# Kernel tuning notes

Measured on AMD Instinct MI355X. Metric: run time of the kernel, lower is better.

The kernel has to match this reference:

```python
import jax, jax.numpy as jnp
from jax import lax
import numpy as np

B, H, W = 8, 36, 100  # stride-8 feature map of 288x800 input
PAD = 4               # ms_ks // 2 for ms_ks = 9
EPS = 1e-5
FC_IN = 5 * (800 // 16) * (288 // 16)  # 4500


def setup_inputs() -> dict:
    key = jax.random.key(0)
    ks = jax.random.split(key, 12)
    r = lambda k, s, sc: jax.random.normal(k, s, jnp.float32) * sc
    return {
        "x": jax.random.normal(ks[0], (B, 512, H, W), jnp.float32),
        "w1a": r(ks[1], (1024, 512, 3, 3), 0.02),
        "bn1_g": jnp.ones(1024, jnp.float32), "bn1_b": jnp.zeros(1024, jnp.float32),
        "bn1_m": jnp.zeros(1024, jnp.float32), "bn1_v": jnp.ones(1024, jnp.float32),
        "w1b": r(ks[2], (128, 1024, 1, 1), 0.03),
        "bn2_g": jnp.ones(128, jnp.float32), "bn2_b": jnp.zeros(128, jnp.float32),
        "bn2_m": jnp.zeros(128, jnp.float32), "bn2_v": jnp.ones(128, jnp.float32),
        "w_ud": r(ks[3], (128, 128, 9), 0.02),
        "w_du": r(ks[4], (128, 128, 9), 0.02),
        "w_lr": r(ks[5], (128, 128, 9), 0.02),
        "w_rl": r(ks[6], (128, 128, 9), 0.02),
        "w2": r(ks[7], (5, 128, 1, 1), 0.05), "b2": jnp.zeros(5, jnp.float32),
        "fc1_w": r(ks[8], (128, FC_IN), 0.02), "fc1_b": jnp.zeros(128, jnp.float32),
        "fc2_w": r(ks[9], (4, 128), 0.05), "fc2_b": jnp.zeros(4, jnp.float32),
    }


def bn(x, g, b, m, v):
    s = (g / jnp.sqrt(v + EPS))
    return x * s[None, :, None, None] + (b - m * s)[None, :, None, None]


def conv2d(x, w, padding, dilation=(1, 1)):
    return lax.conv_general_dilated(x, w, (1, 1), padding, rhs_dilation=dilation,
                                    dimension_numbers=("NCHW", "OIHW", "NCHW"))


def conv1d(x, w):  # x [B,C,L], w [O,I,K]
    return lax.conv_general_dilated(x, w, (1,), [(PAD, PAD)],
                                    dimension_numbers=("NCH", "OIH", "NCH"))


def message_pass(x, w, axis, reverse):
    # x [B,C,H,W]; scan over `axis`, 1D conv along the other spatial dim
    xs = jnp.moveaxis(x, axis, 0)  # [L, B, C, other]
    if reverse:
        xs = xs[::-1]

    def step(prev, cur):
        new = cur + jax.nn.relu(conv1d(prev, w))
        return new, new

    first = xs[0]
    _, rest = lax.scan(step, first, xs[1:])
    out = jnp.concatenate([first[None], rest], axis=0)
    if reverse:
        out = out[::-1]
    return jnp.moveaxis(out, 0, axis)


def upsample_bilinear_ac(x, scale):
    # align_corners=True bilinear, NCHW
    b, c, h, w = x.shape
    ho, wo = h * scale, w * scale

    def grid(n_in, n_out):
        pos = jnp.arange(n_out, dtype=x.dtype) * ((n_in - 1) / (n_out - 1))
        i0 = jnp.clip(jnp.floor(pos).astype(jnp.int32), 0, n_in - 2)
        return i0, pos - i0.astype(x.dtype)

    i0, fh = grid(h, ho)
    j0, fw = grid(w, wo)
    xh = x[:, :, i0, :] * (1 - fh)[None, None, :, None] + x[:, :, i0 + 1, :] * fh[None, None, :, None]
    return xh[:, :, :, j0] * (1 - fw)[None, None, None, :] + xh[:, :, :, j0 + 1] * fw[None, None, None, :]


def reference(x, w1a, bn1_g, bn1_b, bn1_m, bn1_v, w1b, bn2_g, bn2_b, bn2_m, bn2_v,
              w_ud, w_du, w_lr, w_rl, w2, b2, fc1_w, fc1_b, fc2_w, fc2_b):
    # layer1: dilated 3x3 (pad=4, dil=4) -> BN -> ReLU -> 1x1 -> BN -> ReLU
    h = jax.nn.relu(bn(conv2d(x, w1a, [(4, 4), (4, 4)], dilation=(4, 4)), bn1_g, bn1_b, bn1_m, bn1_v))
    h = jax.nn.relu(bn(conv2d(h, w1b, [(0, 0), (0, 0)]), bn2_g, bn2_b, bn2_m, bn2_v))
    # message passing: up-down, down-up (vertical), left-right, right-left (horizontal)
    h = message_pass(h, w_ud, axis=2, reverse=False)
    h = message_pass(h, w_du, axis=2, reverse=True)
    h = message_pass(h, w_lr, axis=3, reverse=False)
    h = message_pass(h, w_rl, axis=3, reverse=True)
    # layer2 (Dropout2d is identity at eval): 1x1 conv -> 5 channels
    h = conv2d(h, w2, [(0, 0), (0, 0)]) + b2[None, :, None, None]
    seg_pred = upsample_bilinear_ac(h, 8)  # [B,5,288,800]
    # layer3: softmax over channels, then AvgPool2d(2,2)
    p = jax.nn.softmax(h, axis=1)
    b_, c_, hh, ww = p.shape
    p = p.reshape(b_, c_, hh // 2, 2, ww // 2, 2).mean(axis=(3, 5))
    # fc: flatten -> 128 -> ReLU -> 4 -> Sigmoid
    f = p.reshape(b_, -1)
    f = jax.nn.relu(f @ fc1_w.T + fc1_b)
    exist_pred = jax.nn.sigmoid(f @ fc2_w.T + fc2_b)
    return seg_pred, exist_pred
```

## Files before the change

### kernel.cpp

```cpp
#include <hip/hip_runtime.h>
#include <hip/hip_bf16.h>
#include <stdint.h>

typedef __bf16 bf16;
typedef bf16 bf16x8 __attribute__((ext_vector_type(8)));
typedef bf16 bf16x4 __attribute__((ext_vector_type(4)));
typedef float f32x4 __attribute__((ext_vector_type(4)));

#define NB 8
#define NH 36
#define NW 100
#define YS 44
#define XSZ 108
#define PIX 28800

#define AS1 __attribute__((address_space(1)))
#define AS3 __attribute__((address_space(3)))

__device__ __forceinline__ void g2l16(const bf16* g, bf16* l) {
    __builtin_amdgcn_global_load_lds((const AS1 void*)g, (AS3 void*)l, 16, 0, 0);
}

static constexpr size_t OFF_XP = 0;
static constexpr size_t SZ_XP  = (size_t)NB*YS*XSZ*512*2;
static constexpr size_t OFF_HP = OFF_XP + SZ_XP;
static constexpr size_t SZ_HP  = (size_t)NB*YS*XSZ*128*2;
static constexpr size_t OFF_A1 = OFF_HP + SZ_HP;
static constexpr size_t SZ_A1  = (size_t)1024*4608*2;
static constexpr size_t OFF_A2 = OFF_A1 + SZ_A1;
static constexpr size_t SZ_A2  = (size_t)128*1024*2;
static constexpr size_t OFF_AW = OFF_A2 + SZ_A2;
static constexpr size_t SZ_AW  = (size_t)4*9*128*128*2;
static constexpr size_t OFF_H1 = OFF_AW + SZ_AW;
static constexpr size_t SZ_H1  = (size_t)PIX*1024*2;
static constexpr size_t OFF_S1 = OFF_H1 + SZ_H1;
static constexpr size_t OFF_T1 = OFF_S1 + 4096;
static constexpr size_t OFF_S2 = OFF_T1 + 4096;
static constexpr size_t OFF_T2 = OFF_S2 + 512;
static constexpr size_t OFF_H5 = OFF_T2 + 512;
static constexpr size_t SZ_H5  = (size_t)NB*5*3600*4;
static constexpr size_t OFF_P  = OFF_H5 + SZ_H5;
static constexpr size_t OFF_F  = OFF_P + SZ_H5;
static constexpr size_t OFF_G  = OFF_F + 144128;
static constexpr size_t OFF_BAR = OFF_G + 4096;

__global__ __launch_bounds__(256) void zero_k(uint4* __restrict__ p, int n) {
    int i = blockIdx.x * 256 + threadIdx.x;
    if (i < n) p[i] = uint4{0u, 0u, 0u, 0u};
}

__global__ __launch_bounds__(256) void prep_x(const float* __restrict__ x, bf16* __restrict__ xp) {
    int bid = blockIdx.x;
    int xc = bid & 3;  int r = bid >> 2;
    int cc = r & 15;   r >>= 4;
    int yo = r % 36;   int b = r / 36;
    int ci0 = cc * 32, xo0 = xc * 32;
    int wdt = 100 - xo0; if (wdt > 32) wdt = 32;
    __shared__ bf16 T[32 * 33];
    int t = threadIdx.x;
    int cl = t >> 5, xl = t & 31;
    if (xl < wdt) {
#pragma unroll
        for (int i = 0; i < 4; i++) {
            int ci = ci0 + cl + 8 * i;
            T[(cl + 8 * i) * 33 + xl] = (bf16)x[((size_t)(b * 512 + ci) * 36 + yo) * 100 + xo0 + xl];
        }
    }
    __syncthreads();
    if (t < 128) {
        int xo2 = t >> 2, oct = t & 3;
        if (xo2 < wdt) {
            bf16x8 vv;
#pragma unroll
            for (int j = 0; j < 8; j++) vv[j] = T[(oct * 8 + j) * 33 + xo2];
            *(bf16x8*)(xp + ((size_t)((b * YS + yo + 4) * XSZ) + xo0 + xo2 + 4) * 512 + ci0 + oct * 8) = vv;
        }
    }
}

__global__ __launch_bounds__(256) void prep_w1a(const float* __restrict__ w, bf16* __restrict__ A) {
    int co = blockIdx.x;
    __shared__ bf16 Wl[4608];
    const float* src = w + (size_t)co * 4608;
    for (int v = threadIdx.x; v < 4608; v += 256) Wl[v] = (bf16)src[v];
    __syncthreads();
    bf16* dst = A + (size_t)co * 4608;
    for (int v = threadIdx.x; v < 4608; v += 256) {
        int rr = v >> 9, ci = v & 511;
        dst[v] = Wl[ci * 9 + rr];
    }
}

__global__ __launch_bounds__(256) void prep_w1b(const float* __restrict__ w, bf16* __restrict__ A) {
    int i = blockIdx.x * 256 + threadIdx.x;
    if (i < 131072) A[i] = (bf16)w[i];
}

__global__ __launch_bounds__(256) void prep_msg(const float* __restrict__ w0, const float* __restrict__ w1,
                                                const float* __restrict__ w2m, const float* __restrict__ w3,
                                                bf16* __restrict__ Aw) {
    int idx = blockIdx.x * 256 + threadIdx.x;
    if (idx >= 4 * 147456) return;
    int w = idx / 147456, r = idx % 147456;
    int t9 = r / 16384, r2 = r % 16384;
    int co = r2 >> 7, ci = r2 & 127;
    const float* s = (w == 0) ? w0 : (w == 1) ? w1 : (w == 2) ? w2m : w3;
    Aw[idx] = (bf16)s[(co * 128 + ci) * 9 + t9];
}

__global__ __launch_bounds__(256) void prep_bn(const float* g1, const float* b1, const float* m1, const float* v1,
                                               const float* g2, const float* b2i, const float* m2, const float* v2,
                                               float* s1, float* t1, float* s2, float* t2,
                                               unsigned* bar) {
    int i = blockIdx.x * 256 + threadIdx.x;
    if (i < 1024) {
        float s = g1[i] / sqrtf(v1[i] + 1e-5f);
        s1[i] = s; t1[i] = b1[i] - m1[i] * s;
    } else if (i < 1152) {
        int c = i - 1024;
        float s = g2[c] / sqrtf(v2[c] + 1e-5f);
        s2[c] = s; t2[c] = b2i[c] - m2[c] * s;
    } else if (i < 1160) {
        bar[i - 1152] = 0u;
    }
}

__device__ __forceinline__ void c1_koff(int ch, int& k0, int& xoff) {
    int ky = ch / 48, rem = ch - ky * 48;
    int kx = rem >> 4, c0 = (rem & 15) << 5;
    k0 = (ky * 3 + kx) * 512 + c0;
    xoff = (ky * XSZ + kx) * 2048 + c0;
}

__device__ __forceinline__ bf16x8 lds_frag(const bf16* S, int row, int q) {
    return *(const bf16x8*)(S + row * 32 + (((q ^ (row >> 1)) & 3) * 8));
}

__global__ __launch_bounds__(256) void conv1_gemm(const bf16* __restrict__ A, const bf16* __restrict__ xp,
                                                  const float* __restrict__ s1, const float* __restrict__ t1,
                                                  bf16* __restrict__ h1) {
    __shared__ __align__(16) bf16 SH[17408];
    bf16* As = SH;
    bf16* Bs = SH + 4096;
    const int t = threadIdx.x;
    const int pt = blockIdx.x, ct = blockIdx.y;
    const int co0 = ct * 128, p0 = pt * 128;
    const int wid = t >> 6, lane = t & 63;

    int aOff[2], bOff[2], ldsOff[2];
#pragma unroll
    for (int j = 0; j < 2; j++) {
        int p = wid * 128 + j * 64 + lane;
        int row = p >> 2;
        int oc = (p & 3) ^ ((p >> 3) & 3);
        aOff[j] = (co0 + row) * 4608 + oc * 8;
        int px = p0 + row;
        int b = px / 3600, rr = px % 3600;
        int y = rr / 100, xx = rr % 100;
        bOff[j] = ((b * YS + y) * XSZ + xx) * 512 + oc * 8;
        ldsOff[j] = (wid * 128 + j * 64) * 8;
    }

    const int mbase = (wid & 1) * 64, nbase = (wid >> 1) * 64;
    const int l15 = lane & 15, q = lane >> 4;

    f32x4 acc[4][4];
#pragma unroll
    for (int i = 0; i < 4; i++)
#pragma unroll
        for (int j = 0; j < 4; j++) acc[i][j] = f32x4{0.f, 0.f, 0.f, 0.f};

    for (int ch = 0; ch < 144; ch++) {
        int k0, xoff;
        c1_koff(ch, k0, xoff);
        __syncthreads();
#pragma unroll
        for (int j = 0; j < 2; j++) {
            g2l16(A + aOff[j] + k0, As + ldsOff[j]);
            g2l16(xp + bOff[j] + xoff, Bs + ldsOff[j]);
        }
        __syncthreads();
        bf16x8 af[4], bfv[4];
#pragma unroll
        for (int mt = 0; mt < 4; mt++) af[mt] = lds_frag(As, mbase + mt * 16 + l15, q);
#pragma unroll
        for (int nt = 0; nt < 4; nt++) bfv[nt] = lds_frag(Bs, nbase + nt * 16 + l15, q);
#pragma unroll
        for (int mt = 0; mt < 4; mt++)
#pragma unroll
            for (int nt = 0; nt < 4; nt++)
                acc[mt][nt] = __builtin_amdgcn_mfma_f32_16x16x32_bf16(af[mt], bfv[nt], acc[mt][nt], 0, 0, 0);
    }

    __syncthreads();
#pragma unroll
    for (int mt = 0; mt < 4; mt++) {
        int co = co0 + mbase + mt * 16 + q * 4;
        f32x4 sc = *(const f32x4*)(s1 + co);
        f32x4 tc = *(const f32x4*)(t1 + co);
#pragma unroll
        for (int nt = 0; nt < 4; nt++) {
            int pxl = nbase + nt * 16 + l15;
            bf16x4 o;
#pragma unroll
            for (int r = 0; r < 4; r++) {
                float v = acc[mt][nt][r] * sc[r] + tc[r];
                o[r] = (bf16)(v > 0.f ? v : 0.f);
            }
            *(bf16x4*)(SH + pxl * 136 + mbase + mt * 16 + q * 4) = o;
        }
    }
    __syncthreads();
#pragma unroll
    for (int i = 0; i < 8; i++) {
        int v = t + 256 * i;
        int pxl = v >> 4, c16 = v & 15;
        *(uint4*)(h1 + (size_t)(p0 + pxl) * 1024 + co0 + c16 * 8) = *(const uint4*)(SH + pxl * 136 + c16 * 8);
    }
}

__global__ __launch_bounds__(256) void conv2_gemm(const bf16* __restrict__ A2, const bf16* __restrict__ h1,
                                                  const float* __restrict__ s2, const float* __restrict__ t2,
                                                  bf16* __restrict__ hp) {
    __shared__ __align__(16) bf16 SH[17408];
    bf16* As = SH;
    bf16* Bs = SH + 4096;
    const int t = threadIdx.x;
    const int p0 = blockIdx.x * 128;
    const int wid = t >> 6, lane = t & 63;

    int aOff[2], bOff[2], ldsOff[2];
#pragma unroll
    for (int j = 0; j < 2; j++) {
        int p = wid * 128 + j * 64 + lane;
        int row = p >> 2;
        int oc = (p & 3) ^ ((p >> 3) & 3);
        aOff[j] = row * 1024 + oc * 8;
        bOff[j] = (p0 + row) * 1024 + oc * 8;
        ldsOff[j] = (wid * 128 + j * 64) * 8;
    }
    const int mbase = (wid & 1) * 64, nbase = (wid >> 1) * 64;
    const int l15 = lane & 15, q = lane >> 4;

    f32x4 acc[4][4];
#pragma unroll
    for (int i = 0; i < 4; i++)
#pragma unroll
        for (int j = 0; j < 4; j++) acc[i][j] = f32x4{0.f, 0.f, 0.f, 0.f};

    for (int ch = 0; ch < 32; ch++) {
        int k0 = ch * 32;
        __syncthreads();
#pragma unroll
        for (int j = 0; j < 2; j++) {
            g2l16(A2 + aOff[j] + k0, As + ldsOff[j]);
            g2l16(h1 + bOff[j] + k0, Bs + ldsOff[j]);
        }
        __syncthreads();
        bf16x8 af[4], bfv[4];
#pragma unroll
        for (int mt = 0; mt < 4; mt++) af[mt] = lds_frag(As, mbase + mt * 16 + l15, q);
#pragma unroll
        for (int nt = 0; nt < 4; nt++) bfv[nt] = lds_frag(Bs, nbase + nt * 16 + l15, q);
#pragma unroll
        for (int mt = 0; mt < 4; mt++)
#pragma unroll
            for (int nt = 0; nt < 4; nt++)
                acc[mt][nt] = __builtin_amdgcn_mfma_f32_16x16x32_bf16(af[mt], bfv[nt], acc[mt][nt], 0, 0, 0);
    }

    __syncthreads();
#pragma unroll
    for (int mt = 0; mt < 4; mt++) {
        int co = mbase + mt * 16 + q * 4;
        f32x4 sc = *(const f32x4*)(s2 + co);
        f32x4 tc = *(const f32x4*)(t2 + co);
#pragma unroll
        for (int nt = 0; nt < 4; nt++) {
            int pxl = nbase + nt * 16 + l15;
            bf16x4 o;
#pragma unroll
            for (int r = 0; r < 4; r++) {
                float v = acc[mt][nt][r] * sc[r] + tc[r];
                o[r] = (bf16)(v > 0.f ? v : 0.f);
            }
            *(bf16x4*)(SH + pxl * 136 + co) = o;
        }
    }
    __syncthreads();
#pragma unroll
    for (int i = 0; i < 8; i++) {
        int v = t + 256 * i;
        int pxl = v >> 4, c16 = v & 15;
        int p = p0 + pxl;
        int b = p / 3600, rr = p % 3600;
        int y = rr / 100, xx = rr % 100;
        *(uint4*)(hp + (size_t)((b * YS + y + 4) * XSZ + xx + 4) * 128 + c16 * 8) = *(const uint4*)(SH + pxl * 136 + c16 * 8);
    }
}

__device__ __forceinline__ bf16x8 awfrag2(const bf16* __restrict__ Aw, int ch, int cs, int l15, int q) {
    int t9 = ch >> 2, c0 = (ch & 3) << 5;
    return *(const bf16x8*)(Aw + (size_t)((t9 * 128 + cs * 16 + l15) << 7) + c0 + q * 8);
}

__device__ __forceinline__ void gbar(unsigned* ctr, int target) {
    __syncthreads();
    if (threadIdx.x == 0) {
        __hip_atomic_fetch_add(ctr, 1u, __ATOMIC_RELEASE, __HIP_MEMORY_SCOPE_AGENT);
        while ((int)__hip_atomic_load(ctr, __ATOMIC_ACQUIRE, __HIP_MEMORY_SCOPE_AGENT) < target)
            __builtin_amdgcn_s_sleep(2);
    }
    __syncthreads();
}

template <int AX, int RV>
__device__ void msg_phase2(const bf16* __restrict__ Aw, bf16* __restrict__ hpb,
                           bf16* __restrict__ Rb, unsigned* ctr, int cs, int& ep) {
    constexpr int STEPS = (AX == 2) ? NH : NW;
    constexpr int NLIM  = (AX == 2) ? NW : NH;
    constexpr int NTW   = (AX == 2) ? 2 : 1;
    const int t = threadIdx.x, wid = t >> 6, lane = t & 63, l15 = lane & 15, q = lane >> 4;

    bf16x8 a[36];
#pragma unroll
    for (int ch = 0; ch < 36; ch++) a[ch] = awfrag2(Aw, ch, cs, l15, q);

    const int nb0 = (AX == 2) ? wid * 32 : wid * 16;
    bool act[NTW];
#pragma unroll
    for (int i = 0; i < NTW; i++) act[i] = (nb0 + i * 16) < NLIM;
    const int co = cs * 16 + q * 4;

    for (int s = 1; s < STEPS; s++) {
        int pos = RV ? (STEPS - 1 - s) : s;
        int prv = RV ? pos + 1 : pos - 1;

        if (AX == 2) {
            const bf16* src = hpb + (size_t)(prv + 4) * XSZ * 128;
            for (int v = t; v < 108 * 16; v += 256) {
                int px = v >> 4, c = (v & 15) * 8;
                *(uint4*)(Rb + px * 136 + c) = *(const uint4*)(src + px * 128 + c);
            }
        } else {
            const bf16* src = hpb + (size_t)(prv + 4) * 128;
            for (int v = t; v < 44 * 16; v += 256) {
                int ys = v >> 4, c = (v & 15) * 8;
                *(uint4*)(Rb + ys * 136 + c) = *(const uint4*)(src + (size_t)ys * XSZ * 128 + c);
            }
        }
        __syncthreads();

        f32x4 acc[NTW];
#pragma unroll
        for (int i = 0; i < NTW; i++) acc[i] = f32x4{0.f, 0.f, 0.f, 0.f};
#pragma unroll
        for (int ch = 0; ch < 36; ch++) {
            int t9 = ch >> 2, c0 = (ch & 3) << 5;
#pragma unroll
            for (int i = 0; i < NTW; i++) {
                if (act[i]) {
                    bf16x8 bfv = *(const bf16x8*)(Rb + (nb0 + i * 16 + l15 + t9) * 136 + c0 + q * 8);
                    acc[i] = __builtin_amdgcn_mfma_f32_16x16x32_bf16(a[ch], bfv, acc[i], 0, 0, 0);
                }
            }
        }

#pragma unroll
        for (int i = 0; i < NTW; i++) {
            if (act[i]) {
                int n = nb0 + i * 16 + l15;
                if (n < NLIM) {
                    size_t g = (AX == 2) ? ((size_t)(pos + 4) * XSZ + (n + 4)) * 128 + co
                                         : ((size_t)(n + 4) * XSZ + (pos + 4)) * 128 + co;
                    bf16x4 cur = *(const bf16x4*)(hpb + g);
                    bf16x4 o;
#pragma unroll
                    for (int r = 0; r < 4; r++) {
                        float v = acc[i][r];
                        v = v > 0.f ? v : 0.f;
                        o[r] = (bf16)((float)cur[r] + v);
                    }
                    *(bf16x4*)(hpb + g) = o;
                }
            }
        }
        ep++;
        gbar(ctr, 8 * ep);
    }
}

__global__ __launch_bounds__(256, 1) void msg_fused(const bf16* __restrict__ Aw, bf16* __restrict__ hp,
                                                    unsigned* __restrict__ bar) {
    __shared__ __align__(16) bf16 Rb[120 * 136];
    const int batch = blockIdx.x & 7;
    const int cs = blockIdx.x >> 3;
    bf16* hpb = hp + (size_t)batch * YS * XSZ * 128;
    unsigned* ctr = bar + batch;
    int ep = 0;
    msg_phase2<2, 0>(Aw + 0 * 147456, hpb, Rb, ctr, cs, ep);
    msg_phase2<2, 1>(Aw + 1 * 147456, hpb, Rb, ctr, cs, ep);
    msg_phase2<3, 0>(Aw + 2 * 147456, hpb, Rb, ctr, cs, ep);
    msg_phase2<3, 1>(Aw + 3 * 147456, hpb, Rb, ctr, cs, ep);
}

__global__ __launch_bounds__(256) void conv3_softmax(const bf16* __restrict__ hp, const float* __restrict__ w2,
                                                     const float* __restrict__ b2, float* __restrict__ h5,
                                                     float* __restrict__ Pp) {
    int idx = blockIdx.x * 256 + threadIdx.x;
    if (idx >= PIX) return;
    int b = idx / 3600, rr = idx % 3600;
    int y = rr / 100, xx = rr % 100;
    const bf16* src = hp + ((size_t)(b * YS + y + 4) * XSZ + xx + 4) * 128;
    float a[5] = {b2[0], b2[1], b2[2], b2[3], b2[4]};
    for (int c8 = 0; c8 < 128; c8 += 8) {
        bf16x8 hv = *(const bf16x8*)(src + c8);
#pragma unroll
        for (int j = 0; j < 8; j++) {
            float hf = (float)hv[j];
            int c = c8 + j;
#pragma unroll
            for (int o = 0; o < 5; o++) a[o] += hf * w2[o * 128 + c];
        }
    }
    float mx = a[0];
#pragma unroll
    for (int o = 1; o < 5; o++) mx = a[o] > mx ? a[o] : mx;
    float e[5], sum = 0.f;
#pragma unroll
    for (int o = 0; o < 5; o++) { e[o] = expf(a[o] - mx); sum += e[o]; }
    float inv = 1.f / sum;
#pragma unroll
    for (int o = 0; o < 5; o++) {
        h5[(size_t)(b * 5 + o) * 3600 + rr] = a[o];
        Pp[(size_t)(b * 5 + o) * 3600 + rr] = e[o] * inv;
    }
}

__global__ __launch_bounds__(256) void pool_k(const float* __restrict__ Pp, float* __restrict__ F) {
    int idx = blockIdx.x * 256 + threadIdx.x;
    if (idx >= 36000) return;
    int xxp = idx % 50, r = idx / 50;
    int yyp = r % 18, bj = r / 18;
    int b = bj / 5, j = bj % 5;
    const float* Pb = Pp + (size_t)bj * 3600;
    float v = 0.25f * (Pb[(2 * yyp) * 100 + 2 * xxp] + Pb[(2 * yyp) * 100 + 2 * xxp + 1] +
                       Pb[(2 * yyp + 1) * 100 + 2 * xxp] + Pb[(2 * yyp + 1) * 100 + 2 * xxp + 1]);
    F[(size_t)b * 4500 + j * 900 + yyp * 50 + xxp] = v;
}

__global__ __launch_bounds__(64) void fc1_k(const float* __restrict__ F, const float* __restrict__ w,
                                            const float* __restrict__ bias, float* __restrict__ G) {
    int co = blockIdx.x;
    int lane = threadIdx.x;
    const float* wr = w + (size_t)co * 4500;
    float a[8] = {0.f, 0.f, 0.f, 0.f, 0.f, 0.f, 0.f, 0.f};
    for (int k = lane; k < 4500; k += 64) {
        float wv = wr[k];
#pragma unroll
        for (int b = 0; b < 8; b++) a[b] += wv * F[b * 4500 + k];
    }
#pragma unroll
    for (int b = 0; b < 8; b++) {
        float r = a[b];
        for (int off = 32; off; off >>= 1) r += __shfl_down(r, off);
        if (lane == 0) {
            float v = r + bias[co];
            G[b * 128 + co] = v > 0.f ? v : 0.f;
        }
    }
}

__global__ __launch_bounds__(64) void fc2_k(const float* __restrict__ G, const float* __restrict__ w,
                                            const float* __restrict__ bias, float* __restrict__ out) {
    int t = threadIdx.x;
    if (t >= 32) return;
    int b = t >> 2, j = t & 3;
    float a = bias[j];
    for (int c = 0; c < 128; c++) a += G[b * 128 + c] * w[j * 128 + c];
    out[9216000 + b * 4 + j] = 1.f / (1.f + expf(-a));
}

__global__ __launch_bounds__(256) void upsample_k(const float* __restrict__ h5, float* __restrict__ out) {
    int idx = blockIdx.x * 256 + threadIdx.x;
    if (idx >= 2304000) return;
    int xq = idx % 200, r = idx / 200;
    int yo = r % 288, bj = r / 288;
    const float* src = h5 + (size_t)bj * 3600;
    float py = yo * (35.0f / 287.0f);
    int i0 = (int)py; if (i0 > 34) i0 = 34;
    float fh = py - (float)i0;
    const float* r0 = src + i0 * 100;
    const float* r1 = r0 + 100;
    float4 o;
    float res[4];
#pragma unroll
    for (int e = 0; e < 4; e++) {
        int xo = xq * 4 + e;
        float px = xo * (99.0f / 799.0f);
        int j0 = (int)px; if (j0 > 98) j0 = 98;
        float fw = px - (float)j0;
        float aa = r0[j0] * (1.f - fh) + r1[j0] * fh;
        float bb = r0[j0 + 1] * (1.f - fh) + r1[j0 + 1] * fh;
        res[e] = aa * (1.f - fw) + bb * fw;
    }
    o.x = res[0]; o.y = res[1]; o.z = res[2]; o.w = res[3];
    *(float4*)(out + (size_t)idx * 4) = o;
}

extern "C" void kernel_launch(void* const* d_in, const int* in_sizes, int n_in,
                              void* d_out, int out_size, void* d_ws, size_t ws_size,
                              hipStream_t stream) {
    (void)in_sizes; (void)n_in; (void)out_size; (void)ws_size;
    const float* x    = (const float*)d_in[0];
    const float* w1a  = (const float*)d_in[1];
    const float* bn1g = (const float*)d_in[2];
    const float* bn1b = (const float*)d_in[3];
    const float* bn1m = (const float*)d_in[4];
    const float* bn1v = (const float*)d_in[5];
    const float* w1b  = (const float*)d_in[6];
    const float* bn2g = (const float*)d_in[7];
    const float* bn2b = (const float*)d_in[8];
    const float* bn2m = (const float*)d_in[9];
    const float* bn2v = (const float*)d_in[10];
    const float* wud  = (const float*)d_in[11];
    const float* wdu  = (const float*)d_in[12];
    const float* wlr  = (const float*)d_in[13];
    const float* wrl  = (const float*)d_in[14];
    const float* w2   = (const float*)d_in[15];
    const float* b2   = (const float*)d_in[16];
    const float* fc1w = (const float*)d_in[17];
    const float* fc1b = (const float*)d_in[18];
    const float* fc2w = (const float*)d_in[19];
    const float* fc2b = (const float*)d_in[20];
    float* out = (float*)d_out;
    char* ws = (char*)d_ws;
    bf16* xp = (bf16*)(ws + OFF_XP);
    bf16* hp = (bf16*)(ws + OFF_HP);
    bf16* A1 = (bf16*)(ws + OFF_A1);
    bf16* A2 = (bf16*)(ws + OFF_A2);
    bf16* Aw = (bf16*)(ws + OFF_AW);
    bf16* h1 = (bf16*)(ws + OFF_H1);
    float* s1 = (float*)(ws + OFF_S1);
    float* t1 = (float*)(ws + OFF_T1);
    float* s2 = (float*)(ws + OFF_S2);
    float* t2 = (float*)(ws + OFF_T2);
    float* h5 = (float*)(ws + OFF_H5);
    float* Pp = (float*)(ws + OFF_P);
    float* Ff = (float*)(ws + OFF_F);
    float* Gg = (float*)(ws + OFF_G);
    unsigned* bar = (unsigned*)(ws + OFF_BAR);

    int nzero = (int)((SZ_XP + SZ_HP) / 16);
    zero_k<<<(nzero + 255) / 256, 256, 0, stream>>>((uint4*)ws, nzero);
    prep_x<<<18432, 256, 0, stream>>>(x, xp);
    prep_w1a<<<1024, 256, 0, stream>>>(w1a, A1);
    prep_w1b<<<512, 256, 0, stream>>>(w1b, A2);
    prep_msg<<<2304, 256, 0, stream>>>(wud, wdu, wlr, wrl, Aw);
    prep_bn<<<5, 256, 0, stream>>>(bn1g, bn1b, bn1m, bn1v, bn2g, bn2b, bn2m, bn2v, s1, t1, s2, t2, bar);

    conv1_gemm<<<dim3(225, 8), 256, 0, stream>>>(A1, xp, s1, t1, h1);
    conv2_gemm<<<225, 256, 0, stream>>>(A2, h1, s2, t2, hp);

    msg_fused<<<64, 256, 0, stream>>>(Aw, hp, bar);

    conv3_softmax<<<113, 256, 0, stream>>>(hp, w2, b2, h5, Pp);
    pool_k<<<141, 256, 0, stream>>>(Pp, Ff);
    fc1_k<<<128, 64, 0, stream>>>(Ff, fc1w, fc1b, Gg);
    fc2_k<<<1, 64, 0, stream>>>(Gg, fc2w, fc2b, out);
    upsample_k<<<9000, 256, 0, stream>>>(h5, out);
}
```

Measured before the change: 2.121 ms.

## Run message passing per batch in one workgroup with LDS double buffering

The message-passing kernel now launches 8 workgroups of 512 threads, one per batch, in place of 64 workgroups split across channel slices. Each of the 8 waves owns a 16-output-channel slice. Because all channels live in one workgroup, the per-step global atomic barrier is replaced by __syncthreads. Each step's output is written into a second LDS buffer that is ping-ponged, so the previous row no longer has to be reloaded from global memory. The trade-off is far less parallelism (8 CUs instead of 64) and more MFMA work per wave per step.

```diff
diff --git a/kernel.cpp b/kernel.cpp
--- a/kernel.cpp
+++ b/kernel.cpp
@@ -6,6 +6,7 @@
 typedef bf16 bf16x8 __attribute__((ext_vector_type(8)));
 typedef bf16 bf16x4 __attribute__((ext_vector_type(4)));
 typedef float f32x4 __attribute__((ext_vector_type(4)));
+typedef unsigned long long u64;
 
 #define NB 8
 #define NH 36
@@ -304,104 +305,104 @@
     return *(const bf16x8*)(Aw + (size_t)((t9 * 128 + cs * 16 + l15) << 7) + c0 + q * 8);
 }
 
-__device__ __forceinline__ void gbar(unsigned* ctr, int target) {
-    __syncthreads();
-    if (threadIdx.x == 0) {
-        __hip_atomic_fetch_add(ctr, 1u, __ATOMIC_RELEASE, __HIP_MEMORY_SCOPE_AGENT);
-        while ((int)__hip_atomic_load(ctr, __ATOMIC_ACQUIRE, __HIP_MEMORY_SCOPE_AGENT) < target)
-            __builtin_amdgcn_s_sleep(2);
-    }
-    __syncthreads();
-}
-
 template <int AX, int RV>
-__device__ void msg_phase2(const bf16* __restrict__ Aw, bf16* __restrict__ hpb,
-                           bf16* __restrict__ Rb, unsigned* ctr, int cs, int& ep) {
+__device__ void phase1cu(const bf16* __restrict__ Aw, bf16* __restrict__ hpb,
+                         bf16*& bp, bf16*& bn) {
     constexpr int STEPS = (AX == 2) ? NH : NW;
     constexpr int NLIM  = (AX == 2) ? NW : NH;
-    constexpr int NTW   = (AX == 2) ? 2 : 1;
+    constexpr int NT    = (AX == 2) ? 7 : 3;
     const int t = threadIdx.x, wid = t >> 6, lane = t & 63, l15 = lane & 15, q = lane >> 4;
 
     bf16x8 a[36];
 #pragma unroll
-    for (int ch = 0; ch < 36; ch++) a[ch] = awfrag2(Aw, ch, cs, l15, q);
-
-    const int nb0 = (AX == 2) ? wid * 32 : wid * 16;
-    bool act[NTW];
-#pragma unroll
-    for (int i = 0; i < NTW; i++) act[i] = (nb0 + i * 16) < NLIM;
-    const int co = cs * 16 + q * 4;
+    for (int ch = 0; ch < 36; ch++) a[ch] = awfrag2(Aw, ch, wid, l15, q);
+
+    const int co = wid * 16 + q * 4;
+    const int pos0 = RV ? (STEPS - 1) : 0;
+
+    if (AX == 2) {
+        const bf16* src = hpb + (size_t)(pos0 + 4) * XSZ * 128;
+        for (int v = t; v < XSZ * 16; v += 512) {
+            int px = v >> 4, c = (v & 15) * 8;
+            *(uint4*)(bp + px * 136 + c) = *(const uint4*)(src + px * 128 + c);
+        }
+    } else {
+        for (int v = t; v < 2 * 16 * 17; v += 512) {
+            int bsel = v >= 272;
+            int r2 = v - bsel * 272;
+            bf16* dst = bsel ? bn : bp;
+            *(uint4*)(dst + (40 + (r2 / 17)) * 136 + (r2 % 17) * 8) = uint4{0u, 0u, 0u, 0u};
+        }
+        const bf16* src = hpb + (size_t)(pos0 + 4) * 128;
+        for (int v = t; v < 40 * 16; v += 512) {
+            int ys = v >> 4, c = (v & 15) * 8;
+            *(uint4*)(bp + ys * 136 + c) = *(const uint4*)(src + (size_t)ys * XSZ * 128 + c);
+        }
+    }
+    __syncthreads();
 
     for (int s = 1; s < STEPS; s++) {
-        int pos = RV ? (STEPS - 1 - s) : s;
-        int prv = RV ? pos + 1 : pos - 1;
-
-        if (AX == 2) {
-            const bf16* src = hpb + (size_t)(prv + 4) * XSZ * 128;
-            for (int v = t; v < 108 * 16; v += 256) {
-                int px = v >> 4, c = (v & 15) * 8;
-                *(uint4*)(Rb + px * 136 + c) = *(const uint4*)(src + px * 128 + c);
+        const int pos = RV ? (STEPS - 1 - s) : s;
+
+        int goff[NT];
+        u64 curv[NT];
+#pragma unroll
+        for (int i = 0; i < NT; i++) {
+            int n = i * 16 + l15;
+            goff[i] = (AX == 2) ? ((pos + 4) * XSZ + n + 4) * 128 + co
+                                : ((n + 4) * XSZ + pos + 4) * 128 + co;
+            curv[i] = 0;
+            if (n < NLIM) curv[i] = *(const u64*)(hpb + goff[i]);
+        }
+
+        f32x4 acc[NT];
+#pragma unroll
+        for (int i = 0; i < NT; i++) acc[i] = f32x4{0.f, 0.f, 0.f, 0.f};
+#pragma unroll
+        for (int ch = 0; ch < 36; ch++) {
+            const int t9 = ch >> 2, c0 = (ch & 3) << 5;
+            const bf16* base = bp + (l15 + t9) * 136 + c0 + q * 8;
+#pragma unroll
+            for (int i = 0; i < NT; i++) {
+                bf16x8 bfv = *(const bf16x8*)(base + i * 16 * 136);
+                acc[i] = __builtin_amdgcn_mfma_f32_16x16x32_bf16(a[ch], bfv, acc[i], 0, 0, 0);
             }
-        } else {
-            const bf16* src = hpb + (size_t)(prv + 4) * 128;
-            for (int v = t; v < 44 * 16; v += 256) {
-                int ys = v >> 4, c = (v & 15) * 8;
-                *(uint4*)(Rb + ys * 136 + c) = *(const uint4*)(src + (size_t)ys * XSZ * 128 + c);
+        }
+
+#pragma unroll
+        for (int i = 0; i < NT; i++) {
+            int n = i * 16 + l15;
+            if (n < NLIM) {
+                bf16x4 cur = *(bf16x4*)&curv[i];
+                bf16x4 o;
+#pragma unroll
+                for (int r = 0; r < 4; r++) {
+                    float v = acc[i][r];
+                    v = v > 0.f ? v : 0.f;
+                    o[r] = (bf16)((float)cur[r] + v);
+                }
+                *(u64*)(hpb + goff[i]) = *(u64*)&o;
+                *(u64*)(bn + (n + 4) * 136 + co) = *(u64*)&o;
             }
         }
         __syncthreads();
-
-        f32x4 acc[NTW];
-#pragma unroll
-        for (int i = 0; i < NTW; i++) acc[i] = f32x4{0.f, 0.f, 0.f, 0.f};
-#pragma unroll
-        for (int ch = 0; ch < 36; ch++) {
-            int t9 = ch >> 2, c0 = (ch & 3) << 5;
-#pragma unroll
-            for (int i = 0; i < NTW; i++) {
-                if (act[i]) {
-                    bf16x8 bfv = *(const bf16x8*)(Rb + (nb0 + i * 16 + l15 + t9) * 136 + c0 + q * 8);
-                    acc[i] = __builtin_amdgcn_mfma_f32_16x16x32_bf16(a[ch], bfv, acc[i], 0, 0, 0);
-                }
-            }
-        }
-
-#pragma unroll
-        for (int i = 0; i < NTW; i++) {
-            if (act[i]) {
-                int n = nb0 + i * 16 + l15;
-                if (n < NLIM) {
-                    size_t g = (AX == 2) ? ((size_t)(pos + 4) * XSZ + (n + 4)) * 128 + co
-                                         : ((size_t)(n + 4) * XSZ + (pos + 4)) * 128 + co;
-                    bf16x4 cur = *(const bf16x4*)(hpb + g);
-                    bf16x4 o;
-#pragma unroll
-                    for (int r = 0; r < 4; r++) {
-                        float v = acc[i][r];
-                        v = v > 0.f ? v : 0.f;
-                        o[r] = (bf16)((float)cur[r] + v);
-                    }
-                    *(bf16x4*)(hpb + g) = o;
-                }
-            }
-        }
-        ep++;
-        gbar(ctr, 8 * ep);
-    }
-}
-
-__global__ __launch_bounds__(256, 1) void msg_fused(const bf16* __restrict__ Aw, bf16* __restrict__ hp,
-                                                    unsigned* __restrict__ bar) {
-    __shared__ __align__(16) bf16 Rb[120 * 136];
-    const int batch = blockIdx.x & 7;
-    const int cs = blockIdx.x >> 3;
+        bf16* tmp = bp; bp = bn; bn = tmp;
+    }
+}
+
+__global__ __launch_bounds__(512, 2) void msg_fused(const bf16* __restrict__ Aw, bf16* __restrict__ hp) {
+    __shared__ __align__(16) bf16 BUF[2][120 * 136];
+    const int batch = blockIdx.x;
     bf16* hpb = hp + (size_t)batch * YS * XSZ * 128;
-    unsigned* ctr = bar + batch;
-    int ep = 0;
-    msg_phase2<2, 0>(Aw + 0 * 147456, hpb, Rb, ctr, cs, ep);
-    msg_phase2<2, 1>(Aw + 1 * 147456, hpb, Rb, ctr, cs, ep);
-    msg_phase2<3, 0>(Aw + 2 * 147456, hpb, Rb, ctr, cs, ep);
-    msg_phase2<3, 1>(Aw + 3 * 147456, hpb, Rb, ctr, cs, ep);
+    for (int v = threadIdx.x; v < 2 * 120 * 17; v += 512)
+        ((uint4*)BUF)[v] = uint4{0u, 0u, 0u, 0u};
+    __syncthreads();
+    bf16* bp = BUF[0];
+    bf16* bn = BUF[1];
+    phase1cu<2, 0>(Aw + 0 * 147456, hpb, bp, bn);
+    phase1cu<2, 1>(Aw + 1 * 147456, hpb, bp, bn);
+    phase1cu<3, 0>(Aw + 2 * 147456, hpb, bp, bn);
+    phase1cu<3, 1>(Aw + 3 * 147456, hpb, bp, bn);
 }
 
 __global__ __launch_bounds__(256) void conv3_softmax(const bf16* __restrict__ hp, const float* __restrict__ w2,
@@ -562,7 +563,7 @@
     conv1_gemm<<<dim3(225, 8), 256, 0, stream>>>(A1, xp, s1, t1, h1);
     conv2_gemm<<<225, 256, 0, stream>>>(A2, h1, s2, t2, hp);
 
-    msg_fused<<<64, 256, 0, stream>>>(Aw, hp, bar);
+    msg_fused<<<8, 512, 0, stream>>>(Aw, hp);
 
     conv3_softmax<<<113, 256, 0, stream>>>(hp, w2, b2, h5, Pp);
     pool_k<<<141, 256, 0, stream>>>(Pp, Ff);
```

After: 1.951 ms. 8.0% less time.
